# Optimization experiments

Measured on AMD Instinct MI355X. Metric: run time of the kernel, lower is better.

The kernel has to match this reference:

```python
import jax, jax.numpy as jnp
import numpy as np

# SMPL-H kintree parents for the first 22 joints (kintree_table[0][:22]); root parent is unused.
SMPL_PARENT = np.array([0, 0, 0, 0, 1, 2, 3, 4, 5, 6, 7, 8, 9, 9, 9, 12, 13, 14, 16, 17, 18, 19], dtype=np.int64)

EPS = 1e-12


def _sixd2matrot(d6):
    # d6: [..., 6] -> R: [..., 3, 3] (rows b1,b2,b3), pytorch3d rotation_6d_to_matrix convention
    a1, a2 = d6[..., :3], d6[..., 3:]
    b1 = a1 / jnp.maximum(jnp.linalg.norm(a1, axis=-1, keepdims=True), EPS)
    a2p = a2 - jnp.sum(b1 * a2, axis=-1, keepdims=True) * b1
    b2 = a2p / jnp.maximum(jnp.linalg.norm(a2p, axis=-1, keepdims=True), EPS)
    b3 = jnp.cross(b1, b2)
    return jnp.stack([b1, b2, b3], axis=-2)


def setup_inputs() -> dict:
    key = jax.random.key(0)
    B, T, J = 512, 196, 22
    pred_pose = jax.random.normal(key, (B, T, J * 6), dtype=jnp.float32)
    return {"pred_pose": pred_pose, "parent": SMPL_PARENT}


def reference(pred_pose, parent):
    B, T, C = pred_pose.shape  # C = 22*6
    J = C // 6
    parent = np.asarray(parent)  # static tree structure
    d6 = pred_pose.reshape(B * T, J, 6)
    R_local = _sixd2matrot(d6)  # [N, J, 3, 3]
    # forward kinematics along the tree: R_global[i] = R_global[parent[i]] @ R_local[i]
    R_global = [R_local[:, 0]]
    for i in range(1, J):
        R_global.append(jnp.einsum('nij,njk->nik', R_global[int(parent[i])], R_local[:, i]))
    R_global = jnp.stack(R_global, axis=1)  # [N, J, 3, 3]
    # matrot -> 6d: first two rows flattened
    rotation_global_r6d = R_global[..., :2, :].reshape(B, T, J * 6)
    return rotation_global_r6d
```

## Files before the change

kernel.cpp:

```cpp
#include <hip/hip_runtime.h>


#define TPB 64
#define TILE_FRAMES 28
#define TILE_FLOATS (TILE_FRAMES * 132)

__device__ __forceinline__ void local_rot(const float* s, float* L) {
    float a1x = s[0], a1y = s[1], a1z = s[2];
    float a2x = s[3], a2y = s[4], a2z = s[5];
    float n1 = sqrtf(a1x * a1x + a1y * a1y + a1z * a1z);
    float i1 = 1.0f / fmaxf(n1, 1e-12f);
    float b1x = a1x * i1, b1y = a1y * i1, b1z = a1z * i1;
    float dt = b1x * a2x + b1y * a2y + b1z * a2z;
    float cx = a2x - dt * b1x, cy = a2y - dt * b1y, cz = a2z - dt * b1z;
    float n2 = sqrtf(cx * cx + cy * cy + cz * cz);
    float i2 = 1.0f / fmaxf(n2, 1e-12f);
    L[0] = b1x; L[1] = b1y; L[2] = b1z;
    L[3] = cx * i2; L[4] = cy * i2; L[5] = cz * i2;
    L[6] = L[1] * L[5] - L[2] * L[4];
    L[7] = L[2] * L[3] - L[0] * L[5];
    L[8] = L[0] * L[4] - L[1] * L[3];
}

__device__ __forceinline__ void matmul3(float* G, const float* P, const float* L) {
#pragma unroll
    for (int r = 0; r < 3; ++r)
#pragma unroll
        for (int c = 0; c < 3; ++c)
            G[3 * r + c] = P[3 * r + 0] * L[0 + c] +
                           P[3 * r + 1] * L[3 + c] +
                           P[3 * r + 2] * L[6 + c];
}

__global__ __launch_bounds__(TPB) void fk6d_kernel(const float* __restrict__ in,
                                                   float* __restrict__ out)
{
    __shared__ float lds[TILE_FLOATS];
    const int lane = threadIdx.x;
    const int half = lane >> 5;
    const int fi = lane & 31;
    const bool act = (fi < TILE_FRAMES);

    const float* gin = in + (size_t)blockIdx.x * TILE_FLOATS;
    float* gout = out + (size_t)blockIdx.x * TILE_FLOATS;

#pragma unroll
    for (int k = 0; k < 14; ++k)
        __builtin_amdgcn_global_load_lds(
            (const __attribute__((address_space(1))) void*)(gin + k * 256 + lane * 4),
            (__attribute__((address_space(3))) void*)(lds + k * 256), 16, 0, 0);
    if (lane < TILE_FRAMES)
        __builtin_amdgcn_global_load_lds(
            (const __attribute__((address_space(1))) void*)(gin + 3584 + lane * 4),
            (__attribute__((address_space(3))) void*)(lds + 3584), 16, 0, 0);
    __syncthreads();

    float* base = lds + fi * 132;
    const float* src = base + 66 * half;

    float L[11][9];
    if (act) {
#pragma unroll
        for (int i = 0; i < 11; ++i) local_rot(src + 6 * i, L[i]);
    }

    float e8[9], e9[9];
    if (act && half == 0) {
        float Rg[11][9];
#pragma unroll
        for (int k = 0; k < 9; ++k) Rg[0][k] = L[0][k];
        matmul3(Rg[1], Rg[0], L[1]);
        matmul3(Rg[2], Rg[0], L[2]);
        matmul3(Rg[3], Rg[0], L[3]);
        matmul3(Rg[4], Rg[1], L[4]);
        matmul3(Rg[5], Rg[2], L[5]);
        matmul3(Rg[6], Rg[3], L[6]);
        matmul3(Rg[7], Rg[4], L[7]);
        matmul3(Rg[8], Rg[5], L[8]);
        matmul3(Rg[9], Rg[6], L[9]);
        matmul3(Rg[10], Rg[7], L[10]);
#pragma unroll
        for (int i = 0; i < 11; ++i)
#pragma unroll
            for (int k = 0; k < 6; ++k) base[6 * i + k] = Rg[i][k];
#pragma unroll
        for (int k = 0; k < 9; ++k) { e8[k] = Rg[8][k]; e9[k] = Rg[9][k]; }
    }

#pragma unroll
    for (int k = 0; k < 9; ++k) {
        e8[k] = __shfl_xor(e8[k], 32, 64);
        e9[k] = __shfl_xor(e9[k], 32, 64);
    }

    if (act && half == 1) {
        float Rg[11][9];
        matmul3(Rg[0], e8, L[0]);
        matmul3(Rg[1], e9, L[1]);
        matmul3(Rg[2], e9, L[2]);
        matmul3(Rg[3], e9, L[3]);
        matmul3(Rg[4], Rg[1], L[4]);
        matmul3(Rg[5], Rg[2], L[5]);
        matmul3(Rg[6], Rg[3], L[6]);
        matmul3(Rg[7], Rg[5], L[7]);
        matmul3(Rg[8], Rg[6], L[8]);
        matmul3(Rg[9], Rg[7], L[9]);
        matmul3(Rg[10], Rg[8], L[10]);
#pragma unroll
        for (int i = 0; i < 11; ++i)
#pragma unroll
            for (int k = 0; k < 6; ++k) base[66 + 6 * i + k] = Rg[i][k];
    }
    __syncthreads();

    const float4* l4 = reinterpret_cast<const float4*>(lds);
    float4* o4 = reinterpret_cast<float4*>(gout);
#pragma unroll
    for (int k = 0; k < 14; ++k) o4[k * 64 + lane] = l4[k * 64 + lane];
    if (lane < TILE_FRAMES) o4[896 + lane] = l4[896 + lane];
}

__global__ void fk6d_tail(const float* __restrict__ in, float* __restrict__ out,
                          int n0, int N) {
    constexpr int PAR[22] = {0, 0, 0, 0, 1, 2, 3, 4, 5, 6, 7, 8, 9, 9, 9,
                             12, 13, 14, 16, 17, 18, 19};
    int n = n0 + blockIdx.x * blockDim.x + threadIdx.x;
    if (n >= N) return;
    const float* src = in + (size_t)n * 132;
    float* dst = out + (size_t)n * 132;
    float Rg[22][9];
#pragma unroll
    for (int j = 0; j < 22; ++j) {
        float Lr[9];
        local_rot(src + 6 * j, Lr);
        if (j == 0) {
#pragma unroll
            for (int k = 0; k < 9; ++k) Rg[0][k] = Lr[k];
        } else {
            matmul3(Rg[j], Rg[PAR[j]], Lr);
        }
#pragma unroll
        for (int k = 0; k < 6; ++k) dst[6 * j + k] = Rg[j][k];
    }
}

extern "C" void kernel_launch(void* const* d_in, const int* in_sizes, int n_in,
                              void* d_out, int out_size, void* d_ws, size_t ws_size,
                              hipStream_t stream) {
    const float* in = (const float*)d_in[0];
    float* out = (float*)d_out;
    int N = in_sizes[0] / 132;
    int NT = N / TILE_FRAMES;
    if (NT > 0) fk6d_kernel<<<NT, TPB, 0, stream>>>(in, out);
    int rem = N - NT * TILE_FRAMES;
    if (rem > 0)
        fk6d_tail<<<(rem + 63) / 64, 64, 0, stream>>>(in, out, NT * TILE_FRAMES, N);
}
```

Baseline: 24.96 us.

## Make FK kernel persistent with double-buffered LDS tile prefetch

The kernel becomes persistent: a fixed grid of 1280 single-wave blocks walks the tiles with a grid stride. Each block keeps two LDS buffers and issues the async global-to-LDS loads for its next tile before computing the current one. Manual s_waitcnt counters replace the barriers. The aim is to overlap input loads with compute and output stores, and to cut per-block launch overhead. In exchange, the doubled LDS footprint lowers the number of resident blocks per CU, and correctness now depends on the hand-tuned vmcnt values.

New measurement: 25.70 us. 2.9% more time.

```diff
diff --git a/kernel.cpp b/kernel.cpp
--- a/kernel.cpp
+++ b/kernel.cpp
@@ -32,30 +32,26 @@
                            P[3 * r + 2] * L[6 + c];
 }
 
-__global__ __launch_bounds__(TPB) void fk6d_kernel(const float* __restrict__ in,
-                                                   float* __restrict__ out)
-{
-    __shared__ float lds[TILE_FLOATS];
-    const int lane = threadIdx.x;
+__device__ __forceinline__ void stage_tile(const float* __restrict__ in,
+                                           int tile, float* buf, int lane) {
+    const float* gin = in + (size_t)tile * TILE_FLOATS;
+#pragma unroll
+    for (int k = 0; k < 14; ++k)
+        __builtin_amdgcn_global_load_lds(
+            (const __attribute__((address_space(1))) void*)(gin + k * 256 + lane * 4),
+            (__attribute__((address_space(3))) void*)(buf + k * 256), 16, 0, 0);
+    if (lane < TILE_FRAMES)
+        __builtin_amdgcn_global_load_lds(
+            (const __attribute__((address_space(1))) void*)(gin + 3584 + lane * 4),
+            (__attribute__((address_space(3))) void*)(buf + 3584), 16, 0, 0);
+}
+
+__device__ __forceinline__ void compute_tile(float* buf, int lane) {
     const int half = lane >> 5;
     const int fi = lane & 31;
     const bool act = (fi < TILE_FRAMES);
 
-    const float* gin = in + (size_t)blockIdx.x * TILE_FLOATS;
-    float* gout = out + (size_t)blockIdx.x * TILE_FLOATS;
-
-#pragma unroll
-    for (int k = 0; k < 14; ++k)
-        __builtin_amdgcn_global_load_lds(
-            (const __attribute__((address_space(1))) void*)(gin + k * 256 + lane * 4),
-            (__attribute__((address_space(3))) void*)(lds + k * 256), 16, 0, 0);
-    if (lane < TILE_FRAMES)
-        __builtin_amdgcn_global_load_lds(
-            (const __attribute__((address_space(1))) void*)(gin + 3584 + lane * 4),
-            (__attribute__((address_space(3))) void*)(lds + 3584), 16, 0, 0);
-    __syncthreads();
-
-    float* base = lds + fi * 132;
+    float* base = buf + fi * 132;
     const float* src = base + 66 * half;
 
     float L[11][9];
@@ -111,13 +107,44 @@
 #pragma unroll
             for (int k = 0; k < 6; ++k) base[66 + 6 * i + k] = Rg[i][k];
     }
-    __syncthreads();
+}
 
-    const float4* l4 = reinterpret_cast<const float4*>(lds);
-    float4* o4 = reinterpret_cast<float4*>(gout);
+__global__ __launch_bounds__(TPB) void fk6d_kernel(const float* __restrict__ in,
+                                                   float* __restrict__ out,
+                                                   int NT, int G)
+{
+    __shared__ float lds[2][TILE_FLOATS];
+    const int lane = threadIdx.x;
+
+    int t = blockIdx.x;
+    if (t < NT) stage_tile(in, t, lds[0], lane);
+
+    int cur = 0;
+    bool first = true;
+    for (; t < NT; t += G) {
+        if (first) {
+            asm volatile("s_waitcnt vmcnt(0)" ::: "memory");
+            first = false;
+        } else {
+            asm volatile("s_waitcnt vmcnt(15)" ::: "memory");
+        }
+
+        int nxt = t + G;
+        if (nxt < NT) stage_tile(in, nxt, lds[cur ^ 1], lane);
+        asm volatile("" ::: "memory");
+
+        compute_tile(lds[cur], lane);
+        asm volatile("s_waitcnt lgkmcnt(0)" ::: "memory");
+
+        float* gdst = out + (size_t)t * TILE_FLOATS;
+        const float4* l4 = reinterpret_cast<const float4*>(lds[cur]);
+        float4* o4 = reinterpret_cast<float4*>(gdst);
 #pragma unroll
-    for (int k = 0; k < 14; ++k) o4[k * 64 + lane] = l4[k * 64 + lane];
-    if (lane < TILE_FRAMES) o4[896 + lane] = l4[896 + lane];
+        for (int k = 0; k < 14; ++k) o4[k * 64 + lane] = l4[k * 64 + lane];
+        if (lane < TILE_FRAMES) o4[896 + lane] = l4[896 + lane];
+
+        cur ^= 1;
+    }
 }
 
 __global__ void fk6d_tail(const float* __restrict__ in, float* __restrict__ out,
@@ -151,7 +178,9 @@
     float* out = (float*)d_out;
     int N = in_sizes[0] / 132;
     int NT = N / TILE_FRAMES;
-    if (NT > 0) fk6d_kernel<<<NT, TPB, 0, stream>>>(in, out);
+    int G = 1280;
+    if (G > NT) G = (NT > 0 ? NT : 1);
+    if (NT > 0) fk6d_kernel<<<G, TPB, 0, stream>>>(in, out, NT, G);
     int rem = N - NT * TILE_FRAMES;
     if (rem > 0)
         fk6d_tail<<<(rem + 63) / 64, 64, 0, stream>>>(in, out, NT * TILE_FRAMES, N);
```
